# Kernel tuning notes

Hardware: AMD Instinct MI355X
Metric: run time of the kernel (lower is better)

Reference implementation:

```python
import jax, jax.numpy as jnp
import numpy as np

D = 256            # number of graph nodes (example.size(3))
K1 = D // 2        # topkpool1 k
K2 = D // 4        # topkpool2 k
B = 8


def _lrelu(x):
    return jnp.where(x > 0, x, 0.33 * x)


def _e2e(h, wa, ba, wb, bb):
    # h: [B,C,d,d]; wa,wb: [P,C,d] (squeezed (1,d)/(d,1) conv kernels)
    # cnn1: contract over columns j -> [B,P,d]; cnn2: contract over rows i -> [B,P,d]
    a = jnp.einsum('bcij,pcj->bpi', h, wa) + ba[None, :, None]
    b = jnp.einsum('bcij,pci->bpj', h, wb) + bb[None, :, None]
    # cat([a]*d, 3) + cat([b]*d, 2)  ==  broadcast-add
    return a[:, :, :, None] + b[:, :, None, :]


def _gcn(h, g, W, b):
    # h: [B,N,F_in], g: [B,N,N]; faithful to norm_g: g[i,j] / deg[j] (column-normalized
    # because torch broadcasts the [N] degree vector over the LAST dim)
    gb = (g > 0).astype(h.dtype)
    deg = gb.sum(axis=2)                      # [B,N] row sums
    gn = gb / deg[:, None, :]                 # divide column j by deg[j]
    return jnp.einsum('bij,bjf->bif', gn, h) @ W.T + b


def _pool(h, g, s, k):
    # h: [B,N,F], g: [B,N,N], s: [B,N,1] -> top-k nodes by score (descending)
    vals, idx = jax.lax.top_k(s[:, :, 0], k)              # [B,k]
    hn = jnp.take_along_axis(h, idx[:, :, None], axis=1)  # [B,k,F]
    gn = jnp.take_along_axis(g, idx[:, :, None], axis=1)
    gn = jnp.take_along_axis(gn, idx[:, None, :], axis=2) # [B,k,k]
    return hn, gn, vals[:, :, None]


def _readout(h):
    # h: [B,N,F] (node axis = 1); torch ReadOut on [B,F,N,1] max/mean over dim=2
    return jnp.concatenate([h.max(axis=1), h.mean(axis=1)], axis=1)  # [B,2F]


def _forward(x, w1a, b1a, w1b, b1b, w2a, b2a, w2b, b2b, e2n_w, e2n_b,
             a11_w, a11_b, a12_w, a12_b, g1_w, g1_b,
             a21_w, a21_b, a22_w, a22_b,
             d1_w, d1_b, d2_w, d2_b, d3_w, d3_b):
    h = _lrelu(_e2e(x, w1a, b1a, w1b, b1b))         # [B,128,d,d]
    h = _lrelu(_e2e(h, w2a, b2a, w2b, b2b))         # [B,256,d,d]
    # E2N conv (1,d): [B,8,d,1] -> node features [B,d,8]
    nodes = _lrelu(jnp.einsum('bcij,pcj->bpi', h, e2n_w) + e2n_b[None, :, None])
    nodes = jnp.transpose(nodes, (0, 2, 1))          # [B,d,8]
    g0 = x[:, 0]                                     # [B,d,d]

    w = _lrelu(_gcn(nodes, g0, a11_w, a11_b))        # [B,d,1]
    w = jax.nn.sigmoid(_gcn(w, g0, a12_w, a12_b))
    h1, g1, s1 = _pool(nodes, g0, w, K1)             # [B,K1,8], [B,K1,K1], [B,K1,1]
    out = h1 * s1 + h1
    sum1 = _readout(out)                             # [B,16]

    h2 = _gcn(out, g1, g1_w, g1_b)                   # [B,K1,8] (no activation, as in torch)
    w = _lrelu(_gcn(h2, g1, a21_w, a21_b))
    w = jax.nn.sigmoid(_gcn(w, g1, a22_w, a22_b))
    h3, g2, s2 = _pool(h2, g1, w, K2)                # [B,K2,8]
    out2 = h3 * s2 + h3
    sum2 = _readout(out2)                            # [B,16]

    z = sum1 + sum2                                  # [B,16]
    z = _lrelu(z @ d1_w.T + d1_b)                    # dropout = identity (eval mode)
    z = _lrelu(z @ d2_w.T + d2_b)
    return z @ d3_w.T + d3_b                         # [B,1]


def setup_inputs() -> dict:
    key = jax.random.key(0)
    ks = jax.random.split(key, 16)
    f32 = jnp.float32

    def rn(k, shape, scale):
        return jax.random.normal(k, shape, dtype=f32) * scale

    return {
        'x': jax.random.normal(ks[0], (B, 1, D, D), dtype=f32),
        'w1a': rn(ks[1], (128, 1, D), 0.08),  'b1a': jnp.zeros((128,), f32),
        'w1b': rn(ks[2], (128, 1, D), 0.08),  'b1b': jnp.zeros((128,), f32),
        'w2a': rn(ks[3], (256, 128, D), 0.008), 'b2a': jnp.zeros((256,), f32),
        'w2b': rn(ks[4], (256, 128, D), 0.008), 'b2b': jnp.zeros((256,), f32),
        'e2n_w': rn(ks[5], (8, 256, D), 0.005), 'e2n_b': jnp.zeros((8,), f32),
        'a11_w': rn(ks[6], (1, 8), 0.3),  'a11_b': jnp.zeros((1,), f32),
        'a12_w': rn(ks[7], (1, 1), 0.3),  'a12_b': jnp.zeros((1,), f32),
        'g1_w': rn(ks[8], (8, 8), 0.3),   'g1_b': jnp.zeros((8,), f32),
        'a21_w': rn(ks[9], (1, 8), 0.3),  'a21_b': jnp.zeros((1,), f32),
        'a22_w': rn(ks[10], (1, 1), 0.3), 'a22_b': jnp.zeros((1,), f32),
        'd1_w': rn(ks[11], (128, 16), 0.2), 'd1_b': jnp.zeros((128,), f32),
        'd2_w': rn(ks[12], (64, 128), 0.08), 'd2_b': jnp.zeros((64,), f32),
        'd3_w': rn(ks[13], (1, 64), 0.1),  'd3_b': jnp.zeros((1,), f32),
    }


def reference(x, w1a, b1a, w1b, b1b, w2a, b2a, w2b, b2b, e2n_w, e2n_b,
              a11_w, a11_b, a12_w, a12_b, g1_w, g1_b,
              a21_w, a21_b, a22_w, a22_b,
              d1_w, d1_b, d2_w, d2_b, d3_w, d3_b):
    return _forward(x, w1a, b1a, w1b, b1b, w2a, b2a, w2b, b2b, e2n_w, e2n_b,
                    a11_w, a11_b, a12_w, a12_b, g1_w, g1_b,
                    a21_w, a21_b, a22_w, a22_b,
                    d1_w, d1_b, d2_w, d2_b, d3_w, d3_b)
```

## Files before the change

### kernel.cpp

```cpp
#include <hip/hip_runtime.h>

typedef short s16x8 __attribute__((ext_vector_type(8)));
typedef float f32x4 __attribute__((ext_vector_type(4)));
typedef float f32x2 __attribute__((ext_vector_type(2)));

#define TID threadIdx.x

__device__ __forceinline__ float lrelu_f(float x) { return fmaxf(x, 0.33f * x); }

__device__ __forceinline__ unsigned lrelu_pack(float pv, f32x2 q) {
    f32x2 s = q + pv;
    f32x2 m = s * 0.33f;
    f32x2 r = __builtin_elementwise_max(s, m);
    unsigned u;
    asm("v_cvt_pk_bf16_f32 %0, %1, %2" : "=v"(u) : "v"(r.x), "v"(r.y));
    return u;
}
__device__ __forceinline__ unsigned pk_bf16(float a, float b) {
    unsigned u;
    asm("v_cvt_pk_bf16_f32 %0, %1, %2" : "=v"(u) : "v"(a), "v"(b));
    return u;
}

union FragU { s16x8 v; uint4 q; unsigned w[4]; };

__global__ __launch_bounds__(256) void k_front(
    const float* __restrict__ x,
    const float* __restrict__ w2a, unsigned short* __restrict__ w2aM,
    const float* __restrict__ w2b, unsigned short* __restrict__ w2bM,
    const float* __restrict__ e2nw, unsigned short* __restrict__ e2nwM,
    const float* __restrict__ w1a, const float* __restrict__ b1a,
    const float* __restrict__ w1b, const float* __restrict__ b1b,
    float* __restrict__ A1, float* __restrict__ B1,
    unsigned long long* __restrict__ adjw, float* __restrict__ rdegw,
    float* __restrict__ nodes_raw)
{
    const int bid = blockIdx.x;
    const int tid = TID;

    __shared__ float xr[2][256];
    __shared__ float xs[64][36];

    if (bid < 1536) {
        const int which = bid >> 9;
        const int inner = bid & 511;
        const float* s; unsigned short* d; int n4;
        if (which == 0)      { s = w2a;  d = w2aM;  n4 = 2097152; }
        else if (which == 1) { s = w2b;  d = w2bM;  n4 = 2097152; }
        else                 { s = e2nw; d = e2nwM; n4 = 131072; }
        for (int i = inner * 256 + tid; i < n4; i += 131072) {
            float4 v = ((const float4*)s)[i];
            ((uint2*)d)[i] = make_uint2(pk_bf16(v.x, v.y), pk_bf16(v.z, v.w));
        }
    } else if (bid < 2560) {
        const int idx = bid - 1536;
        const int rp = idx & 127, b = idx >> 7;
        const int h = tid >> 7, ctid = tid & 127;
        const int r = rp * 2 + h;
        const float* xb = x + b * 65536;
        xr[h][ctid]       = xb[r * 256 + ctid];
        xr[h][ctid + 128] = xb[r * 256 + ctid + 128];
        __syncthreads();
        float acc = b1a[ctid];
        const float* wr = w1a + ctid * 256;
        #pragma unroll 4
        for (int q = 0; q < 256; q += 8) {
            float4 a = *(const float4*)(wr + q);
            float4 c = *(const float4*)(wr + q + 4);
            acc += xr[h][q + 0] * a.x + xr[h][q + 1] * a.y + xr[h][q + 2] * a.z + xr[h][q + 3] * a.w;
            acc += xr[h][q + 4] * c.x + xr[h][q + 5] * c.y + xr[h][q + 6] * c.z + xr[h][q + 7] * c.w;
        }
        A1[b * 32768 + ctid * 256 + r] = acc;
    } else if (bid < 2624) {
        const int idx = bid - 2560;
        const int jt = idx & 7, b = idx >> 3;
        const int c = tid & 127, jh = tid >> 7;
        const float* xb = x + b * 65536;
        float acc[16];
        #pragma unroll
        for (int jj = 0; jj < 16; ++jj) acc[jj] = 0.0f;
        for (int ch = 0; ch < 4; ++ch) {
            const int i0 = ch * 64;
            {
                const int row = tid >> 2, seg = tid & 3;
                const float* src = xb + (i0 + row) * 256 + jt * 32 + seg * 8;
                float4 a0 = *(const float4*)src;
                float4 a1 = *(const float4*)(src + 4);
                *(float4*)&xs[row][seg * 8]     = a0;
                *(float4*)&xs[row][seg * 8 + 4] = a1;
            }
            __syncthreads();
            const float* wrow = w1b + c * 256 + i0;
            #pragma unroll
            for (int i4 = 0; i4 < 64; i4 += 4) {
                float4 wv = *(const float4*)(wrow + i4);
                #pragma unroll
                for (int u = 0; u < 4; ++u) {
                    const float wsc = (u == 0) ? wv.x : (u == 1) ? wv.y : (u == 2) ? wv.z : wv.w;
                    const float* xrow = &xs[i4 + u][jh * 16];
                    #pragma unroll
                    for (int jj = 0; jj < 16; ++jj)
                        acc[jj] += wsc * xrow[jj];
                }
            }
            __syncthreads();
        }
        const float bias = b1b[c];
        float* outp = B1 + b * 32768 + c * 256 + jt * 32 + jh * 16;
        #pragma unroll
        for (int jj = 0; jj < 16; ++jj) outp[jj] = acc[jj] + bias;
    } else {
        const int idx = bid - 2624;
        nodes_raw[idx * 256 + tid] = 0.0f;
        const int gx = idx & 7, b = idx >> 3;
        const int wv = tid >> 6, lane = tid & 63;
        const int rbase = gx * 32 + wv * 8;
        for (int rr = 0; rr < 8; ++rr) {
            const int row = rbase + rr;
            int d = 0;
            unsigned long long w[4];
            #pragma unroll
            for (int k = 0; k < 4; ++k) {
                float v = x[b * 65536 + row * 256 + k * 64 + lane];
                w[k] = __ballot(v > 0.0f);
                d += __popcll(w[k]);
            }
            if (lane == 0) {
                #pragma unroll
                for (int k = 0; k < 4; ++k) adjw[(b * 256 + row) * 4 + k] = w[k];
                rdegw[b * 256 + row] = d ? 1.0f / (float)d : 0.0f;
            }
        }
    }
}

__global__ __launch_bounds__(512, 4) void k_e2e(
    const float* __restrict__ A1, const float* __restrict__ B1,
    const unsigned short* __restrict__ w2aM, const unsigned short* __restrict__ w2bM,
    float* __restrict__ part)
{
    const int bid = blockIdx.x;
    const int xcd = bid & 7, tt = bid >> 3;
    const int hi = tt >> 5, inner = tt & 31;
    const int slice = xcd + 8 * hi;
    const int s = slice >> 1, which = slice & 1;
    const int rt = inner >> 3, b = inner & 7;
    const int bw = b * 2 + which;

    const float* P = (which ? B1 : A1) + b * 32768;
    const float* Q = (which ? A1 : B1) + b * 32768;
    const unsigned short* W = which ? w2bM : w2aM;
    const int c0 = s * 16, r0 = rt * 64;

    __shared__ float Qs[16][256];
    __shared__ float Ps[16][64];
    __shared__ uint4 Hs[2048];

    const int tid = TID;
    const int wave = tid >> 6, lane = tid & 63, quad = lane >> 4, l16 = lane & 15;
    const int pbase = wave * 32;

    {
        const float4* Qg = (const float4*)(Q + c0 * 256);
        float4* Qd = (float4*)&Qs[0][0];
        Qd[tid]       = Qg[tid];
        Qd[tid + 512] = Qg[tid + 512];
        int row = tid >> 5, c2 = (tid & 31) * 2;
        *(float2*)&Ps[row][c2] = *(const float2*)&P[(c0 + row) * 256 + r0 + c2];
    }
    __syncthreads();

    {
        const int qb = wave * 32 + quad * 8;
        f32x2 qp0 = *(const f32x2*)&Qs[0][qb + 0];
        f32x2 qp1 = *(const f32x2*)&Qs[0][qb + 2];
        f32x2 qp2 = *(const f32x2*)&Qs[0][qb + 4];
        f32x2 qp3 = *(const f32x2*)&Qs[0][qb + 6];
        #pragma unroll
        for (int rf = 0; rf < 4; ++rf) {
            float pv = Ps[0][rf * 16 + l16];
            uint4 u;
            u.x = lrelu_pack(pv, qp0);
            u.y = lrelu_pack(pv, qp1);
            u.z = lrelu_pack(pv, qp2);
            u.w = lrelu_pack(pv, qp3);
            Hs[(wave * 4 + rf) * 64 + lane] = u;
        }
    }

    f32x4 acc[2][4] = {};
    const unsigned short* Wrow[2];
    #pragma unroll
    for (int pf = 0; pf < 2; ++pf)
        Wrow[pf] = W + (size_t)(pbase + pf * 16 + l16) * 32768 + c0 * 256 + quad * 8;

    FragU af[2][2];
    #pragma unroll
    for (int pf = 0; pf < 2; ++pf) af[0][pf].q = *(const uint4*)(Wrow[pf]);

    __syncthreads();

    for (int c = 0; c < 16; ++c) {
        FragU hbf[2][4];
        #pragma unroll
        for (int nf = 0; nf < 4; ++nf)
            hbf[0][nf].q = Hs[nf * 64 + lane];

        #pragma unroll
        for (int q0 = 0; q0 < 8; ++q0) {
            const int cur = q0 & 1, nxt = cur ^ 1;
            const int cn = c + ((q0 + 1) >> 3), qn = (q0 + 1) & 7;
            if (cn < 16) {
                #pragma unroll
                for (int pf = 0; pf < 2; ++pf)
                    af[nxt][pf].q = *(const uint4*)(Wrow[pf] + cn * 256 + qn * 32);
            }
            if (q0 < 7) {
                #pragma unroll
                for (int nf = 0; nf < 4; ++nf)
                    hbf[nxt][nf].q = Hs[((q0 + 1) * 4 + nf) * 64 + lane];
            }
            #pragma unroll
            for (int nf = 0; nf < 4; ++nf)
                #pragma unroll
                for (int pf = 0; pf < 2; ++pf)
                    acc[pf][nf] = __builtin_amdgcn_mfma_f32_16x16x32_bf16(af[cur][pf].v, hbf[cur][nf].v, acc[pf][nf], 0, 0, 0);
        }
        __syncthreads();
        if (c + 1 < 16) {
            const int qb = wave * 32 + quad * 8;
            f32x2 qp0 = *(const f32x2*)&Qs[c + 1][qb + 0];
            f32x2 qp1 = *(const f32x2*)&Qs[c + 1][qb + 2];
            f32x2 qp2 = *(const f32x2*)&Qs[c + 1][qb + 4];
            f32x2 qp3 = *(const f32x2*)&Qs[c + 1][qb + 6];
            #pragma unroll
            for (int rf = 0; rf < 4; ++rf) {
                float pv = Ps[c + 1][rf * 16 + l16];
                uint4 u;
                u.x = lrelu_pack(pv, qp0);
                u.y = lrelu_pack(pv, qp1);
                u.z = lrelu_pack(pv, qp2);
                u.w = lrelu_pack(pv, qp3);
                Hs[(wave * 4 + rf) * 64 + lane] = u;
            }
            __syncthreads();
        }
    }

    float* pb = part + (size_t)(s * 16 + bw) * 65536;
    #pragma unroll
    for (int pf = 0; pf < 2; ++pf)
        #pragma unroll
        for (int nf = 0; nf < 4; ++nf)
            #pragma unroll
            for (int t = 0; t < 4; ++t) {
                int p = pbase + pf * 16 + quad * 4 + t;
                int r = r0 + nf * 16 + l16;
                pb[p * 256 + r] = acc[pf][nf][t];
            }
}

__global__ __launch_bounds__(256) void k_red(
    const float* __restrict__ part,
    const float* __restrict__ b2a, const float* __restrict__ b2b,
    float* __restrict__ A2, float* __restrict__ B2)
{
    const int bw = blockIdx.y; const int b = bw >> 1, which = bw & 1;
    const int idx = blockIdx.x * 256 + TID;
    const float4* pp = (const float4*)part;
    float4 acc = make_float4(0.f, 0.f, 0.f, 0.f);
    #pragma unroll
    for (int s = 0; s < 8; ++s) {
        float4 v = pp[(size_t)(s * 16 + bw) * 16384 + idx];
        acc.x += v.x; acc.y += v.y; acc.z += v.z; acc.w += v.w;
    }
    const int p = idx >> 6;
    const float bias = (which ? b2b : b2a)[p];
    acc.x += bias; acc.y += bias; acc.z += bias; acc.w += bias;
    float* OUT = (which ? B2 : A2) + b * 65536;
    ((float4*)OUT)[idx] = acc;
}

__global__ __launch_bounds__(256) void k_e2n(
    const float* __restrict__ A2, const float* __restrict__ B2,
    const unsigned short* __restrict__ e2nw,
    float* __restrict__ nodes_raw)
{
    const int it = blockIdx.x, b = blockIdx.y, sn = blockIdx.z;
    const int tid = TID, wave = tid >> 6, lane = tid & 63, quad = lane >> 4, l16 = lane & 15;
    const int i0 = it * 16;
    const int c0 = sn * 32 + wave * 8;
    const float* Ab = A2 + b * 65536;
    const float* Bb = B2 + b * 65536;
    const float* Brow0 = Bb + c0 * 256 + quad * 8;
    const unsigned short* Wrow0 = e2nw + (size_t)l16 * 65536 + c0 * 256 + quad * 8;

    f32x4 acc = {};
    FragU af[2];
    f32x2 qp[2][4];
    float pv, pvn;

    if (l16 < 8) af[0].q = *(const uint4*)(Wrow0);
    else         af[0].q = make_uint4(0u, 0u, 0u, 0u);
    #pragma unroll
    for (int k = 0; k < 4; ++k) qp[0][k] = *(const f32x2*)(Brow0 + 2 * k);
    pv = Ab[c0 * 256 + i0 + l16];

    for (int cc = 0; cc < 8; ++cc) {
        #pragma unroll
        for (int q0 = 0; q0 < 8; ++q0) {
            const int cur = q0 & 1, nxt = cur ^ 1;
            const int cn = (q0 == 7) ? cc + 1 : cc;
            const int qn = (q0 + 1) & 7;
            if (cn < 8) {
                if (l16 < 8) af[nxt].q = *(const uint4*)(Wrow0 + cn * 256 + qn * 32);
                else         af[nxt].q = make_uint4(0u, 0u, 0u, 0u);
                #pragma unroll
                for (int k = 0; k < 4; ++k)
                    qp[nxt][k] = *(const f32x2*)(Brow0 + cn * 256 + qn * 32 + 2 * k);
            }
            if (q0 == 4 && cc + 1 < 8) pvn = Ab[(c0 + cc + 1) * 256 + i0 + l16];
            FragU hb;
            hb.w[0] = lrelu_pack(pv, qp[cur][0]);
            hb.w[1] = lrelu_pack(pv, qp[cur][1]);
            hb.w[2] = lrelu_pack(pv, qp[cur][2]);
            hb.w[3] = lrelu_pack(pv, qp[cur][3]);
            acc = __builtin_amdgcn_mfma_f32_16x16x32_bf16(af[cur].v, hb.v, acc, 0, 0, 0);
            if (q0 == 7) pv = pvn;
        }
    }
    __shared__ float red[4][16][16];
    #pragma unroll
    for (int t = 0; t < 4; ++t) red[wave][quad * 4 + t][l16] = acc[t];
    __syncthreads();
    const int row = tid >> 4, col = tid & 15;
    if (row < 8) {
        float ssum = red[0][row][col] + red[1][row][col] + red[2][row][col] + red[3][row][col];
        atomicAdd(&nodes_raw[b * 2048 + (i0 + col) * 8 + row], ssum);
    }
}

__global__ __launch_bounds__(256) void k_tail(
    const unsigned long long* __restrict__ adjw, const float* __restrict__ rdegw,
    const float* __restrict__ nodes_raw, const float* __restrict__ e2n_b,
    const float* __restrict__ a11_w, const float* __restrict__ a11_b,
    const float* __restrict__ a12_w, const float* __restrict__ a12_b,
    const float* __restrict__ g1_w,  const float* __restrict__ g1_b,
    const float* __restrict__ a21_w, const float* __restrict__ a21_b,
    const float* __restrict__ a22_w, const float* __restrict__ a22_b,
    const float* __restrict__ d1_w,  const float* __restrict__ d1_b,
    const float* __restrict__ d2_w,  const float* __restrict__ d2_b,
    const float* __restrict__ d3_w,  const float* __restrict__ d3_b,
    float* __restrict__ out)
{
    const int b = blockIdx.x;
    const int tid = TID;

    __shared__ unsigned long long adj[256][4];
    __shared__ float nod[256][8];
    __shared__ float rdeg[256];
    __shared__ float md[256];
    __shared__ float w1s[256];
    __shared__ float w2s[256];
    __shared__ int   selflag[256];
    __shared__ int   selidx[128];
    __shared__ float s1v[128];
    __shared__ float out1[128][8];
    __shared__ float aggL[128][8];
    __shared__ float h2L[128][8];
    __shared__ unsigned long long adj1[128][2];
    __shared__ float rdeg1[128];
    __shared__ float tA[128];
    __shared__ float w1t[128];
    __shared__ float w2t[128];
    __shared__ int   sel2flag[128];
    __shared__ int   sel2idx[64];
    __shared__ float s2v[64];
    __shared__ float out2[64][8];
    __shared__ float r1[16], r2[16], zz[16];
    __shared__ float z1[128];
    __shared__ float z2[64];

    if (tid < 128) { selidx[tid] = 0; s1v[tid] = 0.0f; }
    if (tid < 64)  { sel2idx[tid] = 0; s2v[tid] = 0.0f; }

    {
        #pragma unroll
        for (int k = 0; k < 4; ++k) adj[tid][k] = adjw[(b * 256 + tid) * 4 + k];
        rdeg[tid] = rdegw[b * 256 + tid];
        for (int f = 0; f < 8; ++f)
            nod[tid][f] = lrelu_f(nodes_raw[b * 2048 + tid * 8 + f] + e2n_b[f]);
    }
    __syncthreads();
    {
        float s = 0.0f;
        for (int f = 0; f < 8; ++f) s += nod[tid][f] * a11_w[f];
        md[tid] = s * rdeg[tid];
    }
    __syncthreads();
    {
        float s = 0.0f;
        for (int k = 0; k < 4; ++k) {
            unsigned long long m = adj[tid][k];
            while (m) { int j = __builtin_ctzll(m); m &= m - 1; s += md[k * 64 + j]; }
        }
        w1s[tid] = lrelu_f(s + a11_b[0]);
    }
    __syncthreads();
    md[tid] = w1s[tid] * a12_w[0] * rdeg[tid];
    __syncthreads();
    {
        float s = 0.0f;
        for (int k = 0; k < 4; ++k) {
            unsigned long long m = adj[tid][k];
            while (m) { int j = __builtin_ctzll(m); m &= m - 1; s += md[k * 64 + j]; }
        }
        w2s[tid] = 1.0f / (1.0f + expf(-(s + a12_b[0])));
    }
    __syncthreads();
    {
        const float my = w2s[tid];
        int cnt = 0;
        for (int j = 0; j < 256; ++j) {
            float o = w2s[j];
            cnt += (o > my) || (o == my && j < tid);
        }
        selflag[tid] = (cnt < 128) ? 1 : 0;
    }
    __syncthreads();
    if (selflag[tid]) {
        int pos = 0;
        for (int j = 0; j < tid; ++j) pos += selflag[j];
        if (pos < 128) { selidx[pos] = tid; s1v[pos] = w2s[tid]; }
    }
    __syncthreads();
    for (int k = tid; k < 1024; k += 256) {
        int t = k >> 3, f = k & 7;
        out1[t][f] = nod[selidx[t]][f] * (1.0f + s1v[t]);
    }
    __syncthreads();
    if (tid < 16) {
        int f = tid & 7;
        if (tid < 8) {
            float mx = -INFINITY;
            for (int t = 0; t < 128; ++t) mx = fmaxf(mx, out1[t][f]);
            r1[tid] = mx;
        } else {
            float s = 0.0f;
            for (int t = 0; t < 128; ++t) s += out1[t][f];
            r1[tid] = s * (1.0f / 128.0f);
        }
    }
    if (tid < 128) {
        unsigned long long wds[2] = {0ull, 0ull};
        const int gi = selidx[tid];
        for (int u = 0; u < 128; ++u) {
            const int gj = selidx[u];
            unsigned long long bit = (adj[gi][gj >> 6] >> (gj & 63)) & 1ull;
            wds[u >> 6] |= bit << (u & 63);
        }
        adj1[tid][0] = wds[0]; adj1[tid][1] = wds[1];
        int d = __popcll(wds[0]) + __popcll(wds[1]);
        rdeg1[tid] = d ? 1.0f / (float)d : 0.0f;
    }
    __syncthreads();
    {
        const int t = tid >> 1, f0 = (tid & 1) * 4;
        float a0 = 0, a1 = 0, a2 = 0, a3 = 0;
        for (int k = 0; k < 2; ++k) {
            unsigned long long m = adj1[t][k];
            while (m) {
                int u = __builtin_ctzll(m); m &= m - 1;
                int uu = k * 64 + u;
                float rr = rdeg1[uu];
                a0 += out1[uu][f0 + 0] * rr;
                a1 += out1[uu][f0 + 1] * rr;
                a2 += out1[uu][f0 + 2] * rr;
                a3 += out1[uu][f0 + 3] * rr;
            }
        }
        aggL[t][f0 + 0] = a0; aggL[t][f0 + 1] = a1; aggL[t][f0 + 2] = a2; aggL[t][f0 + 3] = a3;
    }
    __syncthreads();
    for (int k = tid; k < 1024; k += 256) {
        int t = k >> 3, fo = k & 7;
        float s = g1_b[fo];
        for (int f = 0; f < 8; ++f) s += aggL[t][f] * g1_w[fo * 8 + f];
        h2L[t][fo] = s;
    }
    __syncthreads();
    if (tid < 128) {
        float s = 0.0f;
        for (int f = 0; f < 8; ++f) s += h2L[tid][f] * a21_w[f];
        tA[tid] = s * rdeg1[tid];
    }
    __syncthreads();
    if (tid < 128) {
        float s = 0.0f;
        for (int k = 0; k < 2; ++k) {
            unsigned long long m = adj1[tid][k];
            while (m) { int u = __builtin_ctzll(m); m &= m - 1; s += tA[k * 64 + u]; }
        }
        w1t[tid] = lrelu_f(s + a21_b[0]);
    }
    __syncthreads();
    if (tid < 128) tA[tid] = w1t[tid] * a22_w[0] * rdeg1[tid];
    __syncthreads();
    if (tid < 128) {
        float s = 0.0f;
        for (int k = 0; k < 2; ++k) {
            unsigned long long m = adj1[tid][k];
            while (m) { int u = __builtin_ctzll(m); m &= m - 1; s += tA[k * 64 + u]; }
        }
        w2t[tid] = 1.0f / (1.0f + expf(-(s + a22_b[0])));
    }
    __syncthreads();
    if (tid < 128) {
        const float my = w2t[tid];
        int cnt = 0;
        for (int u = 0; u < 128; ++u) {
            float o = w2t[u];
            cnt += (o > my) || (o == my && u < tid);
        }
        sel2flag[tid] = (cnt < 64) ? 1 : 0;
    }
    __syncthreads();
    if (tid < 128 && sel2flag[tid]) {
        int pos = 0;
        for (int u = 0; u < tid; ++u) pos += sel2flag[u];
        if (pos < 64) { sel2idx[pos] = tid; s2v[pos] = w2t[tid]; }
    }
    __syncthreads();
    for (int k = tid; k < 512; k += 256) {
        int u = k >> 3, f = k & 7;
        out2[u][f] = h2L[sel2idx[u]][f] * (1.0f + s2v[u]);
    }
    __syncthreads();
    if (tid < 16) {
        int f = tid & 7;
        if (tid < 8) {
            float mx = -INFINITY;
            for (int t = 0; t < 64; ++t) mx = fmaxf(mx, out2[t][f]);
            r2[tid] = mx;
        } else {
            float s = 0.0f;
            for (int t = 0; t < 64; ++t) s += out2[t][f];
            r2[tid] = s * (1.0f / 64.0f);
        }
    }
    __syncthreads();
    if (tid < 16) zz[tid] = r1[tid] + r2[tid];
    __syncthreads();
    if (tid < 128) {
        float s = d1_b[tid];
        for (int k = 0; k < 16; ++k) s += zz[k] * d1_w[tid * 16 + k];
        z1[tid] = lrelu_f(s);
    }
    __syncthreads();
    if (tid < 64) {
        float s = d2_b[tid];
        for (int k = 0; k < 128; ++k) s += z1[k] * d2_w[tid * 128 + k];
        z2[tid] = lrelu_f(s);
    }
    __syncthreads();
    if (tid == 0) {
        float s = d3_b[0];
        for (int k = 0; k < 64; ++k) s += z2[k] * d3_w[k];
        out[b] = s;
    }
}

extern "C" void kernel_launch(void* const* d_in, const int* in_sizes, int n_in,
                              void* d_out, int out_size, void* d_ws, size_t ws_size,
                              hipStream_t stream) {
    const float* x     = (const float*)d_in[0];
    const float* w1a   = (const float*)d_in[1];
    const float* b1a   = (const float*)d_in[2];
    const float* w1b   = (const float*)d_in[3];
    const float* b1b   = (const float*)d_in[4];
    const float* w2a   = (const float*)d_in[5];
    const float* b2a   = (const float*)d_in[6];
    const float* w2b   = (const float*)d_in[7];
    const float* b2b   = (const float*)d_in[8];
    const float* e2nw  = (const float*)d_in[9];

    float* ws        = (float*)d_ws;
    float* A1        = ws;
    float* B1        = ws + 262144;
    float* A2        = ws + 524288;
    float* B2        = ws + 1048576;
    float* nodes_raw = ws + 1572864;
    float* rdegw     = ws + 1589248;
    unsigned long long* adjw = (unsigned long long*)(ws + 1597440);
    float* part      = ws + 1613824;
    unsigned short* w2aM  = (unsigned short*)(ws + 10002432);
    unsigned short* w2bM  = w2aM + 8388608;
    unsigned short* e2nwM = w2bM + 8388608;

    k_front<<<dim3(2688), 256, 0, stream>>>(
        x, w2a, w2aM, w2b, w2bM, e2nw, e2nwM,
        w1a, b1a, w1b, b1b, A1, B1, adjw, rdegw, nodes_raw);
    k_e2e<<<dim3(512), 512, 0, stream>>>(A1, B1, w2aM, w2bM, part);
    k_red<<<dim3(64, 16), 256, 0, stream>>>(part, b2a, b2b, A2, B2);
    k_e2n<<<dim3(16, 8, 8), 256, 0, stream>>>(A2, B2, e2nwM, nodes_raw);
    k_tail<<<dim3(8), 256, 0, stream>>>(adjw, rdegw, nodes_raw, (const float*)d_in[10],
        (const float*)d_in[11], (const float*)d_in[12], (const float*)d_in[13], (const float*)d_in[14],
        (const float*)d_in[15], (const float*)d_in[16], (const float*)d_in[17], (const float*)d_in[18],
        (const float*)d_in[19], (const float*)d_in[20], (const float*)d_in[21], (const float*)d_in[22],
        (const float*)d_in[23], (const float*)d_in[24], (const float*)d_in[25], (const float*)d_in[26],
        (float*)d_out);
}
```

Baseline: 428.1 us.

## Stream e2e weights via direct global-to-LDS loads and regenerate activations in registers

The second-layer e2e kernel now runs 256 threads per block, with each wave computing a 64x64 output tile (4x4 MFMA fragments) instead of 32x64. Weight fragments are double-buffered in LDS through global_load_lds DMA instead of register prefetches. The lrelu(P+Q) bf16 activations are rebuilt in registers every k-step rather than staged once per channel in shared memory. The aim is to cut global load latency and VGPR pressure for weights and raise MFMA density per wave. The cost is a block barrier every k-step, repeated activation arithmetic, and half as many waves available to hide latency.

```diff
diff --git a/kernel.cpp b/kernel.cpp
--- a/kernel.cpp
+++ b/kernel.cpp
@@ -20,6 +20,13 @@
     unsigned u;
     asm("v_cvt_pk_bf16_f32 %0, %1, %2" : "=v"(u) : "v"(a), "v"(b));
     return u;
+}
+
+__device__ __forceinline__ void gload_lds16(const void* g, void* l) {
+    __builtin_amdgcn_global_load_lds(
+        (const __attribute__((address_space(1))) unsigned*)g,
+        (__attribute__((address_space(3))) unsigned*)l,
+        16, 0, 0);
 }
 
 union FragU { s16x8 v; uint4 q; unsigned w[4]; };
@@ -134,7 +141,7 @@
     }
 }
 
-__global__ __launch_bounds__(512, 4) void k_e2e(
+__global__ __launch_bounds__(256) void k_e2e(
     const float* __restrict__ A1, const float* __restrict__ B1,
     const unsigned short* __restrict__ w2aM, const unsigned short* __restrict__ w2bM,
     float* __restrict__ part)
@@ -154,109 +161,83 @@
 
     __shared__ float Qs[16][256];
     __shared__ float Ps[16][64];
-    __shared__ uint4 Hs[2048];
+    __shared__ uint4 Wl[2][1024];
 
     const int tid = TID;
     const int wave = tid >> 6, lane = tid & 63, quad = lane >> 4, l16 = lane & 15;
-    const int pbase = wave * 32;
 
     {
         const float4* Qg = (const float4*)(Q + c0 * 256);
         float4* Qd = (float4*)&Qs[0][0];
-        Qd[tid]       = Qg[tid];
-        Qd[tid + 512] = Qg[tid + 512];
-        int row = tid >> 5, c2 = (tid & 31) * 2;
-        *(float2*)&Ps[row][c2] = *(const float2*)&P[(c0 + row) * 256 + r0 + c2];
-    }
-    __syncthreads();
-
-    {
-        const int qb = wave * 32 + quad * 8;
-        f32x2 qp0 = *(const f32x2*)&Qs[0][qb + 0];
-        f32x2 qp1 = *(const f32x2*)&Qs[0][qb + 2];
-        f32x2 qp2 = *(const f32x2*)&Qs[0][qb + 4];
-        f32x2 qp3 = *(const f32x2*)&Qs[0][qb + 6];
-        #pragma unroll
-        for (int rf = 0; rf < 4; ++rf) {
-            float pv = Ps[0][rf * 16 + l16];
-            uint4 u;
-            u.x = lrelu_pack(pv, qp0);
-            u.y = lrelu_pack(pv, qp1);
-            u.z = lrelu_pack(pv, qp2);
-            u.w = lrelu_pack(pv, qp3);
-            Hs[(wave * 4 + rf) * 64 + lane] = u;
-        }
-    }
-
-    f32x4 acc[2][4] = {};
-    const unsigned short* Wrow[2];
+        #pragma unroll
+        for (int u = 0; u < 4; ++u) Qd[tid + u * 256] = Qg[tid + u * 256];
+        const int prow = tid >> 4, pc4 = (tid & 15) * 4;
+        *(float4*)&Ps[prow][pc4] = *(const float4*)&P[(c0 + prow) * 256 + r0 + pc4];
+    }
+
+    const int srow = ((tid >> 6) << 4) + (tid & 15);
+    const int skc  = (tid >> 4) & 3;
+    const unsigned short* Wg = W + (size_t)srow * 32768 + c0 * 256 + skc * 8;
+
     #pragma unroll
-    for (int pf = 0; pf < 2; ++pf)
-        Wrow[pf] = W + (size_t)(pbase + pf * 16 + l16) * 32768 + c0 * 256 + quad * 8;
-
-    FragU af[2][2];
-    #pragma unroll
-    for (int pf = 0; pf < 2; ++pf) af[0][pf].q = *(const uint4*)(Wrow[pf]);
-
-    __syncthreads();
-
-    for (int c = 0; c < 16; ++c) {
-        FragU hbf[2][4];
+    for (int u = 0; u < 4; ++u)
+        gload_lds16(Wg + (size_t)u * 64 * 32768, &Wl[0][u * 256 + wave * 64]);
+
+    __syncthreads();
+
+    f32x4 acc[4][4] = {};
+
+    for (int t = 0; t < 128; ++t) {
+        const int cur = t & 1, nxt = cur ^ 1;
+
+        if (t + 1 < 128) {
+            const int cn = (t + 1) >> 3, qn = (t + 1) & 7;
+            const unsigned short* src = Wg + cn * 256 + qn * 32;
+            #pragma unroll
+            for (int u = 0; u < 4; ++u)
+                gload_lds16(src + (size_t)u * 64 * 32768, &Wl[nxt][u * 256 + wave * 64]);
+        }
+
+        const int c = t >> 3, qc = t & 7;
+
+        FragU af[4];
+        #pragma unroll
+        for (int pf = 0; pf < 4; ++pf)
+            af[pf].q = Wl[cur][(wave * 4 + pf) * 64 + lane];
+
+        f32x2 qp[4];
+        #pragma unroll
+        for (int m = 0; m < 4; ++m)
+            qp[m] = *(const f32x2*)&Qs[c][qc * 32 + quad * 8 + 2 * m];
+        FragU hb[4];
+        #pragma unroll
+        for (int nf = 0; nf < 4; ++nf) {
+            const float pv = Ps[c][nf * 16 + l16];
+            hb[nf].w[0] = lrelu_pack(pv, qp[0]);
+            hb[nf].w[1] = lrelu_pack(pv, qp[1]);
+            hb[nf].w[2] = lrelu_pack(pv, qp[2]);
+            hb[nf].w[3] = lrelu_pack(pv, qp[3]);
+        }
+
         #pragma unroll
         for (int nf = 0; nf < 4; ++nf)
-            hbf[0][nf].q = Hs[nf * 64 + lane];
-
-        #pragma unroll
-        for (int q0 = 0; q0 < 8; ++q0) {
-            const int cur = q0 & 1, nxt = cur ^ 1;
-            const int cn = c + ((q0 + 1) >> 3), qn = (q0 + 1) & 7;
-            if (cn < 16) {
-                #pragma unroll
-                for (int pf = 0; pf < 2; ++pf)
-                    af[nxt][pf].q = *(const uint4*)(Wrow[pf] + cn * 256 + qn * 32);
-            }
-            if (q0 < 7) {
-                #pragma unroll
-                for (int nf = 0; nf < 4; ++nf)
-                    hbf[nxt][nf].q = Hs[((q0 + 1) * 4 + nf) * 64 + lane];
-            }
             #pragma unroll
-            for (int nf = 0; nf < 4; ++nf)
-                #pragma unroll
-                for (int pf = 0; pf < 2; ++pf)
-                    acc[pf][nf] = __builtin_amdgcn_mfma_f32_16x16x32_bf16(af[cur][pf].v, hbf[cur][nf].v, acc[pf][nf], 0, 0, 0);
-        }
+            for (int pf = 0; pf < 4; ++pf)
+                acc[pf][nf] = __builtin_amdgcn_mfma_f32_16x16x32_bf16(af[pf].v, hb[nf].v, acc[pf][nf], 0, 0, 0);
+
         __syncthreads();
-        if (c + 1 < 16) {
-            const int qb = wave * 32 + quad * 8;
-            f32x2 qp0 = *(const f32x2*)&Qs[c + 1][qb + 0];
-            f32x2 qp1 = *(const f32x2*)&Qs[c + 1][qb + 2];
-            f32x2 qp2 = *(const f32x2*)&Qs[c + 1][qb + 4];
-            f32x2 qp3 = *(const f32x2*)&Qs[c + 1][qb + 6];
-            #pragma unroll
-            for (int rf = 0; rf < 4; ++rf) {
-                float pv = Ps[c + 1][rf * 16 + l16];
-                uint4 u;
-                u.x = lrelu_pack(pv, qp0);
-                u.y = lrelu_pack(pv, qp1);
-                u.z = lrelu_pack(pv, qp2);
-                u.w = lrelu_pack(pv, qp3);
-                Hs[(wave * 4 + rf) * 64 + lane] = u;
-            }
-            __syncthreads();
-        }
     }
 
     float* pb = part + (size_t)(s * 16 + bw) * 65536;
     #pragma unroll
-    for (int pf = 0; pf < 2; ++pf)
+    for (int pf = 0; pf < 4; ++pf)
         #pragma unroll
         for (int nf = 0; nf < 4; ++nf)
             #pragma unroll
-            for (int t = 0; t < 4; ++t) {
-                int p = pbase + pf * 16 + quad * 4 + t;
+            for (int e = 0; e < 4; ++e) {
+                int p = wave * 64 + pf * 16 + quad * 4 + e;
                 int r = r0 + nf * 16 + l16;
-                pb[p * 256 + r] = acc[pf][nf][t];
+                pb[p * 256 + r] = acc[pf][nf][e];
             }
 }
 
@@ -600,7 +581,7 @@
     k_front<<<dim3(2688), 256, 0, stream>>>(
         x, w2a, w2aM, w2b, w2bM, e2nw, e2nwM,
         w1a, b1a, w1b, b1b, A1, B1, adjw, rdegw, nodes_raw);
-    k_e2e<<<dim3(512), 512, 0, stream>>>(A1, B1, w2aM, w2bM, part);
+    k_e2e<<<dim3(512), 256, 0, stream>>>(A1, B1, w2aM, w2bM, part);
     k_red<<<dim3(64, 16), 256, 0, stream>>>(part, b2a, b2b, A2, B2);
     k_e2n<<<dim3(16, 8, 8), 256, 0, stream>>>(A2, B2, e2nwM, nodes_raw);
     k_tail<<<dim3(8), 256, 0, stream>>>(adjw, rdegw, nodes_raw, (const float*)d_in[10],
```

Result: no change. 435.9 us (+1.8%).
